# Kernel tuning notes

Measured on AMD Instinct MI355X. Metric: run time of the kernel, lower is better.

The kernel has to match this reference:

```python
import jax, jax.numpy as jnp
import numpy as np

SOS, EOS, PAD = 1, 2, 0


def setup_inputs() -> dict:
    key = jax.random.key(0)
    ks = jax.random.split(key, 8)
    n, d_z, d_h, d_emb, V = 8192, 128, 512, 128, 64
    s = lambda k, shape, scale: jax.random.normal(k, shape, jnp.float32) * scale
    return {
        "Z": jax.random.normal(ks[0], (n, d_z), jnp.float32),
        "emb": s(ks[1], (V, d_emb), 0.1),
        "z2h_w": s(ks[2], (d_h, d_z), 0.05),
        "z2h_b": jnp.zeros((d_h,), jnp.float32),
        "w_ih0": s(ks[3], (3 * d_h, d_emb), 0.05),
        "w_ih_rest": s(ks[4], (2, 3 * d_h, d_h), 0.05),
        "w_hh": s(ks[5], (3, 3 * d_h, d_h), 0.05),
        "b_ih": jnp.zeros((3, 3 * d_h), jnp.float32),
        "b_hh": jnp.zeros((3, 3 * d_h), jnp.float32),
        "h2v_w": s(ks[6], (V, d_h), 0.05),
        "h2v_b": jnp.zeros((V,), jnp.float32),
        "max_len": 80,
    }


def _gru_cell(x, h, w_ih, w_hh, b_ih, b_hh):
    # torch GRU gate order: r, z, n
    gi = x @ w_ih.T + b_ih
    gh = h @ w_hh.T + b_hh
    i_r, i_z, i_n = jnp.split(gi, 3, axis=-1)
    h_r, h_z, h_n = jnp.split(gh, 3, axis=-1)
    r = jax.nn.sigmoid(i_r + h_r)
    z = jax.nn.sigmoid(i_z + h_z)
    g = jnp.tanh(i_n + r * h_n)
    return (1.0 - z) * g + z * h


def _decode(Z, emb, z2h_w, z2h_b, w_ih0, w_ih_rest, w_hh, b_ih, b_hh, h2v_w, h2v_b, max_len):
    n = Z.shape[0]
    L = w_hh.shape[0]
    h0 = Z @ z2h_w.T + z2h_b                      # [n, d_h], repeated over layers
    H = jnp.broadcast_to(h0[None], (L,) + h0.shape)
    x0 = jnp.full((n,), SOS, jnp.int32)
    eos0 = jnp.zeros((n,), bool)
    w_ih = [w_ih0] + [w_ih_rest[i] for i in range(w_ih_rest.shape[0])]

    def step(carry, t):
        H, x_prev, eos = carry
        inp = emb[x_prev]                          # [n, d_emb]
        Hs = []
        for l in range(L):                         # small fixed layer loop
            h_new = _gru_cell(inp, H[l], w_ih[l], w_hh[l], b_ih[l], b_hh[l])
            Hs.append(h_new)
            inp = h_new
        probs = jax.nn.softmax(inp @ h2v_w.T + h2v_b, axis=-1)  # [n, V]
        x_t = jnp.argmax(probs, axis=-1).astype(jnp.int32)      # ModeSampler
        tok = jnp.where(eos, PAD, x_t)             # masked write into X_gen
        new_eos = (~eos) & (x_t == EOS)
        return (jnp.stack(Hs), x_t, eos | new_eos), (tok, new_eos, probs)

    ts = jnp.arange(1, max_len, dtype=jnp.int32)
    _, (toks, new_eos, probs) = jax.lax.scan(step, (H, x0, eos0), ts)
    X_gen = jnp.concatenate([jnp.full((n, 1), SOS, jnp.int32), toks.T], axis=1)  # [n, max_len]
    any_eos = new_eos.any(axis=0)
    first_t = ts[jnp.argmax(new_eos, axis=0)]
    seq_lens = jnp.where(any_eos, first_t + 1, max_len).astype(jnp.int32)
    return X_gen, seq_lens, probs


def reference(Z, emb, z2h_w, z2h_b, w_ih0, w_ih_rest, w_hh, b_ih, b_hh, h2v_w, h2v_b, max_len):
    X_gen, seq_lens, _ = _decode(Z, emb, z2h_w, z2h_b, w_ih0, w_ih_rest,
                                 w_hh, b_ih, b_hh, h2v_w, h2v_b, max_len)
    # torch returns a ragged list X_gen[i, :seq_lens[i]]; we return the padded
    # tensor plus lengths (jit-compatible equivalent).
    return X_gen, seq_lens
```

## Files before the change

### kernel.cpp

```cpp
#include <hip/hip_runtime.h>
#include <math.h>

#define NSEQ 8192
#define DH 512
#define DZ 128
#define DE 128
#define VOCAB 64
#define TMAX 80
#define SOS 1
#define EOS_TOK 2

#define TMR 64
#define TNCOL 32

typedef _Float16 half_t;
typedef half_t h8 __attribute__((ext_vector_type(8)));
typedef float f4 __attribute__((ext_vector_type(4)));

__device__ __forceinline__ float sigf(float x) { return 1.0f / (1.0f + expf(-x)); }

__device__ __forceinline__ void split2(float v, half_t& hi, half_t& lo) {
    float hf = (float)(half_t)v;
    if (fabsf(v) < 6.2e-5f) hf = 0.0f;
    hi = (half_t)hf;
    lo = (half_t)((v - hf) * 2048.0f);
}

__device__ __forceinline__ float rec2(half_t h, half_t l) {
    return (float)h + (float)l * (1.0f / 2048.0f);
}

__device__ __forceinline__ void gl_lds16(const void* g, void* l) {
    __builtin_amdgcn_global_load_lds((const __attribute__((address_space(1))) void*)g,
                                     (__attribute__((address_space(3))) void*)l, 16, 0, 0);
}

__device__ __forceinline__ void swizzle_rc(int bid, int& r, int& c) {
    const int x = bid & 7;
    const int q = bid >> 3;
    r = (q & 15) * 8 + x;
    c = q >> 4;
}

__global__ __launch_bounds__(256) void init_kernel(int* __restrict__ x_prev,
                                                   int* __restrict__ eos,
                                                   int* __restrict__ out,
                                                   int* __restrict__ list0,
                                                   int* __restrict__ counts) {
    int i = blockIdx.x * 256 + threadIdx.x;
    x_prev[i] = SOS;
    eos[i] = 0;
    list0[i] = i;
    out[i * TMAX] = SOS;
    out[NSEQ * TMAX + i] = TMAX;
    if (i < TMAX) counts[i] = (i == 0) ? NSEQ : 0;
}

__global__ __launch_bounds__(256) void h0_kernel(const float* __restrict__ Z,
                                                 const float* __restrict__ w,
                                                 const float* __restrict__ b,
                                                 half_t* __restrict__ B0h, half_t* __restrict__ B0l,
                                                 half_t* __restrict__ B1h, half_t* __restrict__ B1l,
                                                 half_t* __restrict__ B2h, half_t* __restrict__ B2l) {
    __shared__ float zrow[DZ];
    const int i = blockIdx.x;
    const int tid = threadIdx.x;
    if (tid < DZ) zrow[tid] = Z[(size_t)i * DZ + tid];
    __syncthreads();
    for (int j = tid; j < DH; j += 256) {
        double s = (double)b[j];
        const float* wr = w + (size_t)j * DZ;
#pragma unroll 8
        for (int k = 0; k < DZ; ++k) s += (double)zrow[k] * (double)wr[k];
        float sf = (float)s;
        half_t hi, lo;
        split2(sf, hi, lo);
        size_t o = (size_t)i * DH + j;
        B0h[o] = hi; B0l[o] = lo;
        B1h[o] = hi; B1l[o] = lo;
        B2h[o] = hi; B2l[o] = lo;
    }
}

__global__ __launch_bounds__(256) void gi0_kernel(const float* __restrict__ emb,
                                                  const float* __restrict__ w_ih0,
                                                  const float* __restrict__ b_ih0,
                                                  double* __restrict__ tab) {
    __shared__ float e[DE];
    const int x = blockIdx.x;
    const int tid = threadIdx.x;
    if (tid < DE) e[tid] = emb[(size_t)x * DE + tid];
    __syncthreads();
    for (int j = tid; j < 3 * DH; j += 256) {
        double s = (double)b_ih0[j];
        const float* wr = w_ih0 + (size_t)j * DE;
#pragma unroll 8
        for (int k = 0; k < DE; ++k) s += (double)e[k] * (double)wr[k];
        tab[(size_t)x * 3 * DH + j] = s;
    }
}

__global__ __launch_bounds__(256) void wsplit_kernel(const float* __restrict__ w,
                                                     half_t* __restrict__ hi,
                                                     half_t* __restrict__ lo, int n) {
    int i = blockIdx.x * 256 + threadIdx.x;
    if (i < n) {
        half_t h, l;
        split2(w[i], h, l);
        hi[i] = h; lo[i] = l;
    }
}


__global__ __launch_bounds__(256, 3) void layer0_mfma(
    const half_t* __restrict__ Hch, const half_t* __restrict__ Hcl,
    half_t* __restrict__ Hnh, half_t* __restrict__ Hnl,
    const half_t* __restrict__ Wh, const half_t* __restrict__ Wl,
    const float* __restrict__ b_hh0,
    const double* __restrict__ tab,
    const int* __restrict__ x_prev,
    const int* __restrict__ list, const int* __restrict__ count) {
    int rt, ct;
    swizzle_rc(blockIdx.x, rt, ct);
    const int row0 = rt * TMR;
    const int cnt = count[0];
    if (row0 >= cnt) return;
    const int col0 = ct * TNCOL;

    __shared__ char sm[40960];
    const int tid = threadIdx.x;
    const int lane = tid & 63, w = tid >> 6;
    const int lr = lane & 15, lq = lane >> 4;
    const int wr0 = (w >> 1) * 32, wc0 = (w & 1) * 16;

    int aoff[2], boff[3];
#pragma unroll
    for (int i = 0; i < 2; ++i) {
        int u = i * 256 + tid, r = u >> 3, s = u & 7;
        int rr = row0 + r; if (rr > cnt - 1) rr = cnt - 1;
        aoff[i] = list[rr] * 1024 + ((s ^ (r & 7)) << 4);
    }
#pragma unroll
    for (int j = 0; j < 3; ++j) {
        int u = j * 256 + tid, br = u >> 3, s = u & 7;
        int wr = (br >> 5) * DH + col0 + (br & 31);
        boff[j] = wr * 1024 + ((s ^ (br & 7)) << 4);
    }

    int fa[2][2], fb[3][2];
#pragma unroll
    for (int rf = 0; rf < 2; ++rf)
#pragma unroll
        for (int ks = 0; ks < 2; ++ks) {
            int row = wr0 + rf * 16 + lr;
            int sb = ks * 4 + lq;
            fa[rf][ks] = row * 128 + ((sb ^ (row & 7)) << 4);
        }
#pragma unroll
    for (int g = 0; g < 3; ++g)
#pragma unroll
        for (int ks = 0; ks < 2; ++ks) {
            int br = g * 32 + wc0 + lr;
            int sb = ks * 4 + lq;
            fb[g][ks] = br * 128 + ((sb ^ (br & 7)) << 4);
        }

    f4 hh[2][3] = {}, cc[2][3] = {};
    const char* Ah = (const char*)Hch;
    const char* Al = (const char*)Hcl;
    const char* Bh = (const char*)Wh;
    const char* Bl = (const char*)Wl;

    for (int kc = 0; kc < 8; ++kc) {
        const int kb = kc * 128;
#pragma unroll
        for (int i = 0; i < 2; ++i) {
            gl_lds16(Ah + aoff[i] + kb, sm + (i * 256 + tid) * 16);
            gl_lds16(Al + aoff[i] + kb, sm + 8192 + (i * 256 + tid) * 16);
        }
#pragma unroll
        for (int j = 0; j < 3; ++j) {
            gl_lds16(Bh + boff[j] + kb, sm + 16384 + (j * 256 + tid) * 16);
            gl_lds16(Bl + boff[j] + kb, sm + 28672 + (j * 256 + tid) * 16);
        }
        __syncthreads();
#pragma unroll
        for (int ks = 0; ks < 2; ++ks) {
            h8 a0h = *(const h8*)(sm + fa[0][ks]);
            h8 a0l = *(const h8*)(sm + 8192 + fa[0][ks]);
            h8 a1h = *(const h8*)(sm + fa[1][ks]);
            h8 a1l = *(const h8*)(sm + 8192 + fa[1][ks]);
#pragma unroll
            for (int g = 0; g < 3; ++g) {
                h8 bh = *(const h8*)(sm + 16384 + fb[g][ks]);
                h8 bl = *(const h8*)(sm + 28672 + fb[g][ks]);
                hh[0][g] = __builtin_amdgcn_mfma_f32_16x16x32_f16(a0h, bh, hh[0][g], 0, 0, 0);
                cc[0][g] = __builtin_amdgcn_mfma_f32_16x16x32_f16(a0h, bl, cc[0][g], 0, 0, 0);
                cc[0][g] = __builtin_amdgcn_mfma_f32_16x16x32_f16(a0l, bh, cc[0][g], 0, 0, 0);
                hh[1][g] = __builtin_amdgcn_mfma_f32_16x16x32_f16(a1h, bh, hh[1][g], 0, 0, 0);
                cc[1][g] = __builtin_amdgcn_mfma_f32_16x16x32_f16(a1h, bl, cc[1][g], 0, 0, 0);
                cc[1][g] = __builtin_amdgcn_mfma_f32_16x16x32_f16(a1l, bh, cc[1][g], 0, 0, 0);
            }
        }
        __syncthreads();
    }

    const float inv = 1.0f / 2048.0f;
#pragma unroll
    for (int rf = 0; rf < 2; ++rf) {
        f4 pR = hh[rf][0] + cc[rf][0] * inv;
        f4 pZ = hh[rf][1] + cc[rf][1] * inv;
        f4 pN = hh[rf][2] + cc[rf][2] * inv;
        const int gj = col0 + wc0 + lr;
#pragma unroll
        for (int reg = 0; reg < 4; ++reg) {
            int pos = row0 + wr0 + rf * 16 + lq * 4 + reg;
            if (pos > cnt - 1) pos = cnt - 1;
            const int gi = list[pos];
            const double* tr = tab + (size_t)x_prev[gi] * (3 * DH);
            float xr = (float)(tr[gj] + (double)pR[reg] + (double)b_hh0[gj]);
            float xz = (float)(tr[DH + gj] + (double)pZ[reg] + (double)b_hh0[DH + gj]);
            float hn_pre = pN[reg] + b_hh0[2 * DH + gj];
            float r = sigf(xr), z = sigf(xz);
            float g = tanhf((float)(tr[2 * DH + gj] + (double)r * (double)hn_pre));
            size_t o = (size_t)gi * DH + gj;
            float ho = rec2(Hch[o], Hcl[o]);
            float h = (1.0f - z) * g + z * ho;
            half_t oh, ol;
            split2(h, oh, ol);
            Hnh[o] = oh; Hnl[o] = ol;
        }
    }
}

__global__ __launch_bounds__(256, 3) void layer12_mfma(
    const half_t* __restrict__ Xh, const half_t* __restrict__ Xl,
    const half_t* __restrict__ Hch, const half_t* __restrict__ Hcl,
    half_t* __restrict__ Hnh, half_t* __restrict__ Hnl,
    const half_t* __restrict__ Wih_h, const half_t* __restrict__ Wih_l,
    const half_t* __restrict__ Whh_h, const half_t* __restrict__ Whh_l,
    const float* __restrict__ b_ih, const float* __restrict__ b_hh,
    const int* __restrict__ list, const int* __restrict__ count) {
    int rt, ct;
    swizzle_rc(blockIdx.x, rt, ct);
    const int row0 = rt * TMR;
    const int cnt = count[0];
    if (row0 >= cnt) return;
    const int col0 = ct * TNCOL;

    __shared__ char sm[40960];
    const int tid = threadIdx.x;
    const int lane = tid & 63, w = tid >> 6;
    const int lr = lane & 15, lq = lane >> 4;
    const int wr0 = (w >> 1) * 32, wc0 = (w & 1) * 16;

    int aoff[2], boff[3];
#pragma unroll
    for (int i = 0; i < 2; ++i) {
        int u = i * 256 + tid, r = u >> 3, s = u & 7;
        int rr = row0 + r; if (rr > cnt - 1) rr = cnt - 1;
        aoff[i] = list[rr] * 1024 + ((s ^ (r & 7)) << 4);
    }
#pragma unroll
    for (int j = 0; j < 3; ++j) {
        int u = j * 256 + tid, br = u >> 3, s = u & 7;
        int wr = (br >> 5) * DH + col0 + (br & 31);
        boff[j] = wr * 1024 + ((s ^ (br & 7)) << 4);
    }

    int fa[2][2], fb[3][2];
#pragma unroll
    for (int rf = 0; rf < 2; ++rf)
#pragma unroll
        for (int ks = 0; ks < 2; ++ks) {
            int row = wr0 + rf * 16 + lr;
            int sb = ks * 4 + lq;
            fa[rf][ks] = row * 128 + ((sb ^ (row & 7)) << 4);
        }
#pragma unroll
    for (int g = 0; g < 3; ++g)
#pragma unroll
        for (int ks = 0; ks < 2; ++ks) {
            int br = g * 32 + wc0 + lr;
            int sb = ks * 4 + lq;
            fb[g][ks] = br * 128 + ((sb ^ (br & 7)) << 4);
        }

    f4 hh[2][3] = {}, cc[2][3] = {}, niS[2] = {};

    for (int kc = 0; kc < 16; ++kc) {
        const int kb = (kc & 7) * 128;
        const char* As_h = (kc < 8) ? (const char*)Xh : (const char*)Hch;
        const char* As_l = (kc < 8) ? (const char*)Xl : (const char*)Hcl;
        const char* Ws_h = (kc < 8) ? (const char*)Wih_h : (const char*)Whh_h;
        const char* Ws_l = (kc < 8) ? (const char*)Wih_l : (const char*)Whh_l;
#pragma unroll
        for (int i = 0; i < 2; ++i) {
            gl_lds16(As_h + aoff[i] + kb, sm + (i * 256 + tid) * 16);
            gl_lds16(As_l + aoff[i] + kb, sm + 8192 + (i * 256 + tid) * 16);
        }
#pragma unroll
        for (int j = 0; j < 3; ++j) {
            gl_lds16(Ws_h + boff[j] + kb, sm + 16384 + (j * 256 + tid) * 16);
            gl_lds16(Ws_l + boff[j] + kb, sm + 28672 + (j * 256 + tid) * 16);
        }
        __syncthreads();
#pragma unroll
        for (int ks = 0; ks < 2; ++ks) {
            h8 a0h = *(const h8*)(sm + fa[0][ks]);
            h8 a0l = *(const h8*)(sm + 8192 + fa[0][ks]);
            h8 a1h = *(const h8*)(sm + fa[1][ks]);
            h8 a1l = *(const h8*)(sm + 8192 + fa[1][ks]);
#pragma unroll
            for (int g = 0; g < 3; ++g) {
                h8 bh = *(const h8*)(sm + 16384 + fb[g][ks]);
                h8 bl = *(const h8*)(sm + 28672 + fb[g][ks]);
                hh[0][g] = __builtin_amdgcn_mfma_f32_16x16x32_f16(a0h, bh, hh[0][g], 0, 0, 0);
                cc[0][g] = __builtin_amdgcn_mfma_f32_16x16x32_f16(a0h, bl, cc[0][g], 0, 0, 0);
                cc[0][g] = __builtin_amdgcn_mfma_f32_16x16x32_f16(a0l, bh, cc[0][g], 0, 0, 0);
                hh[1][g] = __builtin_amdgcn_mfma_f32_16x16x32_f16(a1h, bh, hh[1][g], 0, 0, 0);
                cc[1][g] = __builtin_amdgcn_mfma_f32_16x16x32_f16(a1h, bl, cc[1][g], 0, 0, 0);
                cc[1][g] = __builtin_amdgcn_mfma_f32_16x16x32_f16(a1l, bh, cc[1][g], 0, 0, 0);
            }
        }
        __syncthreads();
        if (kc == 7) {
#pragma unroll
            for (int rf = 0; rf < 2; ++rf) {
                niS[rf] = hh[rf][2] + cc[rf][2] * (1.0f / 2048.0f);
                f4 zz = {0.0f, 0.0f, 0.0f, 0.0f};
                hh[rf][2] = zz;
                cc[rf][2] = zz;
            }
        }
    }

    const float inv = 1.0f / 2048.0f;
#pragma unroll
    for (int rf = 0; rf < 2; ++rf) {
        f4 pR = hh[rf][0] + cc[rf][0] * inv;
        f4 pZ = hh[rf][1] + cc[rf][1] * inv;
        f4 pNH = hh[rf][2] + cc[rf][2] * inv;
        f4 pNI = niS[rf];
        const int gj = col0 + wc0 + lr;
#pragma unroll
        for (int reg = 0; reg < 4; ++reg) {
            int pos = row0 + wr0 + rf * 16 + lq * 4 + reg;
            if (pos > cnt - 1) pos = cnt - 1;
            const int gi = list[pos];
            float xr = pR[reg] + b_ih[gj] + b_hh[gj];
            float xz = pZ[reg] + b_ih[DH + gj] + b_hh[DH + gj];
            float xi = pNI[reg] + b_ih[2 * DH + gj];
            float hn_pre = pNH[reg] + b_hh[2 * DH + gj];
            float r = sigf(xr), z = sigf(xz);
            float g = tanhf(xi + r * hn_pre);
            size_t o = (size_t)gi * DH + gj;
            float ho = rec2(Hch[o], Hcl[o]);
            float h = (1.0f - z) * g + z * ho;
            half_t oh, ol;
            split2(h, oh, ol);
            Hnh[o] = oh; Hnl[o] = ol;
        }
    }
}

__global__ __launch_bounds__(256) void logits_kernel(const half_t* __restrict__ H2h,
                                                     const half_t* __restrict__ H2l,
                                                     const float* __restrict__ h2v_w,
                                                     const float* __restrict__ h2v_b,
                                                     int* __restrict__ x_prev,
                                                     int* __restrict__ eos,
                                                     int* __restrict__ out,
                                                     const int* __restrict__ list,
                                                     const int* __restrict__ count,
                                                     int* __restrict__ list_next,
                                                     int* __restrict__ count_next,
                                                     int t) {
    const int rowbase = blockIdx.x * 16;
    const int cnt = count[0];
    if (rowbase >= cnt) return;

    __shared__ float Ws[VOCAB][65];
    __shared__ float Hs[16][65];
    __shared__ int sact[16];
    const int tid = threadIdx.x;
    double acc[4] = {0.0, 0.0, 0.0, 0.0};

    for (int k0 = 0; k0 < DH; k0 += 64) {
        __syncthreads();
#pragma unroll
        for (int it = 0; it < 16; ++it) {
            int idx = tid + 256 * it;
            int v = idx >> 6, k = idx & 63;
            Ws[v][k] = h2v_w[(size_t)v * DH + k0 + k];
        }
#pragma unroll
        for (int it = 0; it < 4; ++it) {
            int idx = tid + 256 * it;
            int r = idx >> 6, k = idx & 63;
            int pos = rowbase + r; if (pos > cnt - 1) pos = cnt - 1;
            size_t o = (size_t)list[pos] * DH + k0 + k;
            Hs[r][k] = rec2(H2h[o], H2l[o]);
        }
        __syncthreads();
        const int r = tid >> 4;
        const int vb = (tid & 15) * 4;
#pragma unroll 16
        for (int k = 0; k < 64; ++k) {
            double h = (double)Hs[r][k];
            acc[0] += h * (double)Ws[vb + 0][k];
            acc[1] += h * (double)Ws[vb + 1][k];
            acc[2] += h * (double)Ws[vb + 2][k];
            acc[3] += h * (double)Ws[vb + 3][k];
        }
    }

    const int r = tid >> 4;
    const int vb = (tid & 15) * 4;
    float lf[4];
#pragma unroll
    for (int vv = 0; vv < 4; ++vv) lf[vv] = (float)(acc[vv] + (double)h2v_b[vb + vv]);

    float m = fmaxf(fmaxf(lf[0], lf[1]), fmaxf(lf[2], lf[3]));
#pragma unroll
    for (int off = 1; off < 16; off <<= 1) m = fmaxf(m, __shfl_xor(m, off));
    float e[4];
    float ssum = 0.f;
#pragma unroll
    for (int vv = 0; vv < 4; ++vv) { e[vv] = expf(lf[vv] - m); ssum += e[vv]; }
#pragma unroll
    for (int off = 1; off < 16; off <<= 1) ssum += __shfl_xor(ssum, off);

    float best = e[0] / ssum;
    int bi = vb;
#pragma unroll
    for (int vv = 1; vv < 4; ++vv) {
        float pv = e[vv] / ssum;
        if (pv > best) { best = pv; bi = vb + vv; }
    }
#pragma unroll
    for (int off = 1; off < 16; off <<= 1) {
        float ov = __shfl_xor(best, off);
        int oi = __shfl_xor(bi, off);
        if (ov > best || (ov == best && oi < bi)) { best = ov; bi = oi; }
    }
    if ((tid & 15) == 0) {
        const int pos = rowbase + r;
        const bool valid = pos < cnt;
        const int gi = list[valid ? pos : (cnt - 1)];
        const int ee = eos[gi];
        const int xt = bi;
        if (valid) {
            out[(size_t)gi * TMAX + t] = ee ? 0 : xt;
            if (!ee && xt == EOS_TOK) {
                out[NSEQ * TMAX + gi] = t + 1;
                eos[gi] = 1;
            }
            x_prev[gi] = xt;
        }
        sact[r] = (valid && !ee && xt != EOS_TOK) ? gi : -1;
    }
    __syncthreads();
    if (tid == 0) {
        int loc[16], k = 0;
#pragma unroll
        for (int i = 0; i < 16; ++i) { int v = sact[i]; if (v >= 0) loc[k++] = v; }
        if (k > 0) {
            int b = atomicAdd(count_next, k);
            for (int i = 0; i < k; ++i) list_next[b + i] = loc[i];
        }
    }
}

extern "C" void kernel_launch(void* const* d_in, const int* in_sizes, int n_in,
                              void* d_out, int out_size, void* d_ws, size_t ws_size,
                              hipStream_t stream) {
    const float* Z        = (const float*)d_in[0];
    const float* emb      = (const float*)d_in[1];
    const float* z2h_w    = (const float*)d_in[2];
    const float* z2h_b    = (const float*)d_in[3];
    const float* w_ih0    = (const float*)d_in[4];
    const float* w_ih_rest= (const float*)d_in[5];
    const float* w_hh     = (const float*)d_in[6];
    const float* b_ih     = (const float*)d_in[7];
    const float* b_hh     = (const float*)d_in[8];
    const float* h2v_w    = (const float*)d_in[9];
    const float* h2v_b    = (const float*)d_in[10];

    int* out = (int*)d_out;
    char* p = (char*)d_ws;
    const size_t HS = (size_t)NSEQ * DH * sizeof(half_t);
    half_t* Bh[4]; half_t* Bl[4];
    for (int i = 0; i < 4; ++i) { Bh[i] = (half_t*)p; p += HS; }
    for (int i = 0; i < 4; ++i) { Bl[i] = (half_t*)p; p += HS; }
    double* tab = (double*)p; p += (size_t)VOCAB * 3 * DH * sizeof(double);
    const size_t WH = (size_t)3 * DH * DH;
    half_t* wih_h = (half_t*)p; p += 2 * WH * sizeof(half_t);
    half_t* wih_l = (half_t*)p; p += 2 * WH * sizeof(half_t);
    half_t* whh_h = (half_t*)p; p += 3 * WH * sizeof(half_t);
    half_t* whh_l = (half_t*)p; p += 3 * WH * sizeof(half_t);
    int* x_prev = (int*)p; p += NSEQ * sizeof(int);
    int* eos    = (int*)p; p += NSEQ * sizeof(int);
    int* lists[2];
    lists[0] = (int*)p; p += NSEQ * sizeof(int);
    lists[1] = (int*)p; p += NSEQ * sizeof(int);
    int* counts = (int*)p; p += 128 * sizeof(int);

    hipMemsetAsync(out, 0, (size_t)NSEQ * TMAX * sizeof(int), stream);
    init_kernel<<<NSEQ / 256, 256, 0, stream>>>(x_prev, eos, out, lists[0], counts);
    h0_kernel<<<NSEQ, 256, 0, stream>>>(Z, z2h_w, z2h_b,
                                        Bh[0], Bl[0], Bh[1], Bl[1], Bh[2], Bl[2]);
    gi0_kernel<<<VOCAB, 256, 0, stream>>>(emb, w_ih0, b_ih, tab);
    wsplit_kernel<<<(int)((2 * WH + 255) / 256), 256, 0, stream>>>(w_ih_rest, wih_h, wih_l, (int)(2 * WH));
    wsplit_kernel<<<(int)((3 * WH + 255) / 256), 256, 0, stream>>>(w_hh, whh_h, whh_l, (int)(3 * WH));

    int c0 = 0, c1 = 1, c2 = 2, sp = 3;
    const int lgrid = (NSEQ / TMR) * (DH / TNCOL);
    for (int t = 1; t < TMAX; ++t) {
        const int* lcur = lists[(t - 1) & 1];
        const int* ccur = counts + (t - 1);
        layer0_mfma<<<lgrid, 256, 0, stream>>>(Bh[c0], Bl[c0], Bh[sp], Bl[sp],
            whh_h, whh_l, b_hh, tab, x_prev, lcur, ccur);
        layer12_mfma<<<lgrid, 256, 0, stream>>>(Bh[sp], Bl[sp], Bh[c1], Bl[c1], Bh[c0], Bl[c0],
            wih_h, wih_l, whh_h + WH, whh_l + WH, b_ih + 3 * DH, b_hh + 3 * DH, lcur, ccur);
        layer12_mfma<<<lgrid, 256, 0, stream>>>(Bh[c0], Bl[c0], Bh[c2], Bl[c2], Bh[c1], Bl[c1],
            wih_h + WH, wih_l + WH, whh_h + 2 * WH, whh_l + 2 * WH,
            b_ih + 6 * DH, b_hh + 6 * DH, lcur, ccur);
        logits_kernel<<<NSEQ / 16, 256, 0, stream>>>(Bh[c1], Bl[c1], h2v_w, h2v_b,
                                                     x_prev, eos, out, lcur, ccur,
                                                     lists[t & 1], counts + t, t);
        int n0 = sp, n1 = c0, n2 = c1, nsp = c2;
        c0 = n0; c1 = n1; c2 = n2; sp = nsp;
    }
}
```

Baseline: 14.82 ms.

## Double row tile to 128 and interleave hi/lo halves in one LDS tile

Row tile per block grows from 64 to 128, so each wave computes 4 row fragments and reuses each loaded B fragment across more MFMAs. The K chunk shrinks to 32 elements and hi/lo fp16 parts are packed into the same swizzled LDS row, which cuts shared memory from 40KB to 28KB and halves the number of global-to-LDS copy instructions per chunk. In exchange the kernel runs twice as many K iterations with their barriers, needs more accumulator registers (occupancy bound lowered to 2 blocks), and launches half as many row blocks, which hurts load balance when the active count is small.

Measured after the change: 18.69 ms. 26.2% more time.

```diff
diff --git a/kernel.cpp b/kernel.cpp
--- a/kernel.cpp
+++ b/kernel.cpp
@@ -10,7 +10,7 @@
 #define SOS 1
 #define EOS_TOK 2
 
-#define TMR 64
+#define TMR 128
 #define TNCOL 32
 
 typedef _Float16 half_t;
@@ -38,8 +38,8 @@
 __device__ __forceinline__ void swizzle_rc(int bid, int& r, int& c) {
     const int x = bid & 7;
     const int q = bid >> 3;
-    r = (q & 15) * 8 + x;
-    c = q >> 4;
+    r = (q & 7) * 8 + x;
+    c = q >> 3;
 }
 
 __global__ __launch_bounds__(256) void init_kernel(int* __restrict__ x_prev,
@@ -112,7 +112,7 @@
 }
 
 
-__global__ __launch_bounds__(256, 3) void layer0_mfma(
+__global__ __launch_bounds__(256, 2) void layer0_mfma(
     const half_t* __restrict__ Hch, const half_t* __restrict__ Hcl,
     half_t* __restrict__ Hnh, half_t* __restrict__ Hnl,
     const half_t* __restrict__ Wh, const half_t* __restrict__ Wl,
@@ -127,91 +127,85 @@
     if (row0 >= cnt) return;
     const int col0 = ct * TNCOL;
 
-    __shared__ char sm[40960];
+    __shared__ __align__(16) char sm[28672];
     const int tid = threadIdx.x;
     const int lane = tid & 63, w = tid >> 6;
     const int lr = lane & 15, lq = lane >> 4;
-    const int wr0 = (w >> 1) * 32, wc0 = (w & 1) * 16;
-
-    int aoff[2], boff[3];
-#pragma unroll
-    for (int i = 0; i < 2; ++i) {
-        int u = i * 256 + tid, r = u >> 3, s = u & 7;
+    const int wr0 = (w >> 1) * 64, wc0 = (w & 1) * 16;
+
+    int aoff[4], ahi[4];
+#pragma unroll
+    for (int i = 0; i < 4; ++i) {
+        int u = i * 256 + tid, r = u >> 3, p = u & 7;
+        int l = p ^ (r & 7);
         int rr = row0 + r; if (rr > cnt - 1) rr = cnt - 1;
-        aoff[i] = list[rr] * 1024 + ((s ^ (r & 7)) << 4);
-    }
+        aoff[i] = list[rr] * 1024 + (l & 3) * 16;
+        ahi[i] = (l < 4);
+    }
+    int boff[3], bhi[3];
 #pragma unroll
     for (int j = 0; j < 3; ++j) {
-        int u = j * 256 + tid, br = u >> 3, s = u & 7;
-        int wr = (br >> 5) * DH + col0 + (br & 31);
-        boff[j] = wr * 1024 + ((s ^ (br & 7)) << 4);
-    }
-
-    int fa[2][2], fb[3][2];
-#pragma unroll
-    for (int rf = 0; rf < 2; ++rf)
-#pragma unroll
-        for (int ks = 0; ks < 2; ++ks) {
-            int row = wr0 + rf * 16 + lr;
-            int sb = ks * 4 + lq;
-            fa[rf][ks] = row * 128 + ((sb ^ (row & 7)) << 4);
-        }
-#pragma unroll
-    for (int g = 0; g < 3; ++g)
-#pragma unroll
-        for (int ks = 0; ks < 2; ++ks) {
-            int br = g * 32 + wc0 + lr;
-            int sb = ks * 4 + lq;
-            fb[g][ks] = br * 128 + ((sb ^ (br & 7)) << 4);
-        }
-
-    f4 hh[2][3] = {}, cc[2][3] = {};
-    const char* Ah = (const char*)Hch;
-    const char* Al = (const char*)Hcl;
-    const char* Bh = (const char*)Wh;
-    const char* Bl = (const char*)Wl;
-
-    for (int kc = 0; kc < 8; ++kc) {
-        const int kb = kc * 128;
-#pragma unroll
-        for (int i = 0; i < 2; ++i) {
-            gl_lds16(Ah + aoff[i] + kb, sm + (i * 256 + tid) * 16);
-            gl_lds16(Al + aoff[i] + kb, sm + 8192 + (i * 256 + tid) * 16);
-        }
-#pragma unroll
-        for (int j = 0; j < 3; ++j) {
-            gl_lds16(Bh + boff[j] + kb, sm + 16384 + (j * 256 + tid) * 16);
-            gl_lds16(Bl + boff[j] + kb, sm + 28672 + (j * 256 + tid) * 16);
-        }
+        int u = j * 256 + tid, r = u >> 3, p = u & 7;
+        int l = p ^ (r & 7);
+        int wr = (r >> 5) * DH + col0 + (r & 31);
+        boff[j] = wr * 1024 + (l & 3) * 16;
+        bhi[j] = (l < 4);
+    }
+
+    int fah[4], fal[4], fbh[3], fbl[3];
+#pragma unroll
+    for (int rf = 0; rf < 4; ++rf) {
+        int arow = wr0 + rf * 16 + lr;
+        fah[rf] = arow * 128 + ((lq ^ (arow & 7)) << 4);
+        fal[rf] = arow * 128 + (((lq ^ 4) ^ (arow & 7)) << 4);
+    }
+#pragma unroll
+    for (int g = 0; g < 3; ++g) {
+        int brow = g * 32 + wc0 + lr;
+        fbh[g] = 16384 + brow * 128 + ((lq ^ (brow & 7)) << 4);
+        fbl[g] = 16384 + brow * 128 + (((lq ^ 4) ^ (brow & 7)) << 4);
+    }
+
+    f4 hh[4][3] = {}, cc[4][3] = {};
+
+    for (int kc = 0; kc < 16; ++kc) {
+        const int kb = kc * 64;
+#pragma unroll
+        for (int i = 0; i < 4; ++i)
+            gl_lds16((ahi[i] ? (const char*)Hch : (const char*)Hcl) + aoff[i] + kb,
+                     sm + (i * 256 + tid) * 16);
+#pragma unroll
+        for (int j = 0; j < 3; ++j)
+            gl_lds16((bhi[j] ? (const char*)Wh : (const char*)Wl) + boff[j] + kb,
+                     sm + 16384 + (j * 256 + tid) * 16);
         __syncthreads();
-#pragma unroll
-        for (int ks = 0; ks < 2; ++ks) {
-            h8 a0h = *(const h8*)(sm + fa[0][ks]);
-            h8 a0l = *(const h8*)(sm + 8192 + fa[0][ks]);
-            h8 a1h = *(const h8*)(sm + fa[1][ks]);
-            h8 a1l = *(const h8*)(sm + 8192 + fa[1][ks]);
-#pragma unroll
-            for (int g = 0; g < 3; ++g) {
-                h8 bh = *(const h8*)(sm + 16384 + fb[g][ks]);
-                h8 bl = *(const h8*)(sm + 28672 + fb[g][ks]);
-                hh[0][g] = __builtin_amdgcn_mfma_f32_16x16x32_f16(a0h, bh, hh[0][g], 0, 0, 0);
-                cc[0][g] = __builtin_amdgcn_mfma_f32_16x16x32_f16(a0h, bl, cc[0][g], 0, 0, 0);
-                cc[0][g] = __builtin_amdgcn_mfma_f32_16x16x32_f16(a0l, bh, cc[0][g], 0, 0, 0);
-                hh[1][g] = __builtin_amdgcn_mfma_f32_16x16x32_f16(a1h, bh, hh[1][g], 0, 0, 0);
-                cc[1][g] = __builtin_amdgcn_mfma_f32_16x16x32_f16(a1h, bl, cc[1][g], 0, 0, 0);
-                cc[1][g] = __builtin_amdgcn_mfma_f32_16x16x32_f16(a1l, bh, cc[1][g], 0, 0, 0);
+        h8 ah[4], al[4];
+#pragma unroll
+        for (int rf = 0; rf < 4; ++rf) {
+            ah[rf] = *(const h8*)(sm + fah[rf]);
+            al[rf] = *(const h8*)(sm + fal[rf]);
+        }
+#pragma unroll
+        for (int g = 0; g < 3; ++g) {
+            h8 bh = *(const h8*)(sm + fbh[g]);
+            h8 bl = *(const h8*)(sm + fbl[g]);
+#pragma unroll
+            for (int rf = 0; rf < 4; ++rf) {
+                hh[rf][g] = __builtin_amdgcn_mfma_f32_16x16x32_f16(ah[rf], bh, hh[rf][g], 0, 0, 0);
+                cc[rf][g] = __builtin_amdgcn_mfma_f32_16x16x32_f16(ah[rf], bl, cc[rf][g], 0, 0, 0);
+                cc[rf][g] = __builtin_amdgcn_mfma_f32_16x16x32_f16(al[rf], bh, cc[rf][g], 0, 0, 0);
             }
         }
         __syncthreads();
     }
 
     const float inv = 1.0f / 2048.0f;
-#pragma unroll
-    for (int rf = 0; rf < 2; ++rf) {
+    const int gj = col0 + wc0 + lr;
+#pragma unroll
+    for (int rf = 0; rf < 4; ++rf) {
         f4 pR = hh[rf][0] + cc[rf][0] * inv;
         f4 pZ = hh[rf][1] + cc[rf][1] * inv;
         f4 pN = hh[rf][2] + cc[rf][2] * inv;
-        const int gj = col0 + wc0 + lr;
 #pragma unroll
         for (int reg = 0; reg < 4; ++reg) {
             int pos = row0 + wr0 + rf * 16 + lq * 4 + reg;
@@ -233,7 +227,7 @@
     }
 }
 
-__global__ __launch_bounds__(256, 3) void layer12_mfma(
+__global__ __launch_bounds__(256, 2) void layer12_mfma(
     const half_t* __restrict__ Xh, const half_t* __restrict__ Xl,
     const half_t* __restrict__ Hch, const half_t* __restrict__ Hcl,
     half_t* __restrict__ Hnh, half_t* __restrict__ Hnl,
@@ -248,85 +242,81 @@
     if (row0 >= cnt) return;
     const int col0 = ct * TNCOL;
 
-    __shared__ char sm[40960];
+    __shared__ __align__(16) char sm[28672];
     const int tid = threadIdx.x;
     const int lane = tid & 63, w = tid >> 6;
     const int lr = lane & 15, lq = lane >> 4;
-    const int wr0 = (w >> 1) * 32, wc0 = (w & 1) * 16;
-
-    int aoff[2], boff[3];
-#pragma unroll
-    for (int i = 0; i < 2; ++i) {
-        int u = i * 256 + tid, r = u >> 3, s = u & 7;
+    const int wr0 = (w >> 1) * 64, wc0 = (w & 1) * 16;
+
+    int aoff[4], ahi[4];
+#pragma unroll
+    for (int i = 0; i < 4; ++i) {
+        int u = i * 256 + tid, r = u >> 3, p = u & 7;
+        int l = p ^ (r & 7);
         int rr = row0 + r; if (rr > cnt - 1) rr = cnt - 1;
-        aoff[i] = list[rr] * 1024 + ((s ^ (r & 7)) << 4);
-    }
+        aoff[i] = list[rr] * 1024 + (l & 3) * 16;
+        ahi[i] = (l < 4);
+    }
+    int boff[3], bhi[3];
 #pragma unroll
     for (int j = 0; j < 3; ++j) {
-        int u = j * 256 + tid, br = u >> 3, s = u & 7;
-        int wr = (br >> 5) * DH + col0 + (br & 31);
-        boff[j] = wr * 1024 + ((s ^ (br & 7)) << 4);
-    }
-
-    int fa[2][2], fb[3][2];
-#pragma unroll
-    for (int rf = 0; rf < 2; ++rf)
-#pragma unroll
-        for (int ks = 0; ks < 2; ++ks) {
-            int row = wr0 + rf * 16 + lr;
-            int sb = ks * 4 + lq;
-            fa[rf][ks] = row * 128 + ((sb ^ (row & 7)) << 4);
-        }
-#pragma unroll
-    for (int g = 0; g < 3; ++g)
-#pragma unroll
-        for (int ks = 0; ks < 2; ++ks) {
-            int br = g * 32 + wc0 + lr;
-            int sb = ks * 4 + lq;
-            fb[g][ks] = br * 128 + ((sb ^ (br & 7)) << 4);
-        }
-
-    f4 hh[2][3] = {}, cc[2][3] = {}, niS[2] = {};
-
-    for (int kc = 0; kc < 16; ++kc) {
-        const int kb = (kc & 7) * 128;
-        const char* As_h = (kc < 8) ? (const char*)Xh : (const char*)Hch;
-        const char* As_l = (kc < 8) ? (const char*)Xl : (const char*)Hcl;
-        const char* Ws_h = (kc < 8) ? (const char*)Wih_h : (const char*)Whh_h;
-        const char* Ws_l = (kc < 8) ? (const char*)Wih_l : (const char*)Whh_l;
-#pragma unroll
-        for (int i = 0; i < 2; ++i) {
-            gl_lds16(As_h + aoff[i] + kb, sm + (i * 256 + tid) * 16);
-            gl_lds16(As_l + aoff[i] + kb, sm + 8192 + (i * 256 + tid) * 16);
-        }
-#pragma unroll
-        for (int j = 0; j < 3; ++j) {
-            gl_lds16(Ws_h + boff[j] + kb, sm + 16384 + (j * 256 + tid) * 16);
-            gl_lds16(Ws_l + boff[j] + kb, sm + 28672 + (j * 256 + tid) * 16);
-        }
+        int u = j * 256 + tid, r = u >> 3, p = u & 7;
+        int l = p ^ (r & 7);
+        int wr = (r >> 5) * DH + col0 + (r & 31);
+        boff[j] = wr * 1024 + (l & 3) * 16;
+        bhi[j] = (l < 4);
+    }
+
+    int fah[4], fal[4], fbh[3], fbl[3];
+#pragma unroll
+    for (int rf = 0; rf < 4; ++rf) {
+        int arow = wr0 + rf * 16 + lr;
+        fah[rf] = arow * 128 + ((lq ^ (arow & 7)) << 4);
+        fal[rf] = arow * 128 + (((lq ^ 4) ^ (arow & 7)) << 4);
+    }
+#pragma unroll
+    for (int g = 0; g < 3; ++g) {
+        int brow = g * 32 + wc0 + lr;
+        fbh[g] = 16384 + brow * 128 + ((lq ^ (brow & 7)) << 4);
+        fbl[g] = 16384 + brow * 128 + (((lq ^ 4) ^ (brow & 7)) << 4);
+    }
+
+    f4 hh[4][3] = {}, cc[4][3] = {}, niS[4] = {};
+
+    for (int kc = 0; kc < 32; ++kc) {
+        const int kb = (kc & 15) * 64;
+        const char* Ah_ = (kc < 16) ? (const char*)Xh : (const char*)Hch;
+        const char* Al_ = (kc < 16) ? (const char*)Xl : (const char*)Hcl;
+        const char* Wh_ = (kc < 16) ? (const char*)Wih_h : (const char*)Whh_h;
+        const char* Wl_ = (kc < 16) ? (const char*)Wih_l : (const char*)Whh_l;
+#pragma unroll
+        for (int i = 0; i < 4; ++i)
+            gl_lds16((ahi[i] ? Ah_ : Al_) + aoff[i] + kb, sm + (i * 256 + tid) * 16);
+#pragma unroll
+        for (int j = 0; j < 3; ++j)
+            gl_lds16((bhi[j] ? Wh_ : Wl_) + boff[j] + kb, sm + 16384 + (j * 256 + tid) * 16);
         __syncthreads();
-#pragma unroll
-        for (int ks = 0; ks < 2; ++ks) {
-            h8 a0h = *(const h8*)(sm + fa[0][ks]);
-            h8 a0l = *(const h8*)(sm + 8192 + fa[0][ks]);
-            h8 a1h = *(const h8*)(sm + fa[1][ks]);
-            h8 a1l = *(const h8*)(sm + 8192 + fa[1][ks]);
-#pragma unroll
-            for (int g = 0; g < 3; ++g) {
-                h8 bh = *(const h8*)(sm + 16384 + fb[g][ks]);
-                h8 bl = *(const h8*)(sm + 28672 + fb[g][ks]);
-                hh[0][g] = __builtin_amdgcn_mfma_f32_16x16x32_f16(a0h, bh, hh[0][g], 0, 0, 0);
-                cc[0][g] = __builtin_amdgcn_mfma_f32_16x16x32_f16(a0h, bl, cc[0][g], 0, 0, 0);
-                cc[0][g] = __builtin_amdgcn_mfma_f32_16x16x32_f16(a0l, bh, cc[0][g], 0, 0, 0);
-                hh[1][g] = __builtin_amdgcn_mfma_f32_16x16x32_f16(a1h, bh, hh[1][g], 0, 0, 0);
-                cc[1][g] = __builtin_amdgcn_mfma_f32_16x16x32_f16(a1h, bl, cc[1][g], 0, 0, 0);
-                cc[1][g] = __builtin_amdgcn_mfma_f32_16x16x32_f16(a1l, bh, cc[1][g], 0, 0, 0);
+        h8 ah[4], al[4];
+#pragma unroll
+        for (int rf = 0; rf < 4; ++rf) {
+            ah[rf] = *(const h8*)(sm + fah[rf]);
+            al[rf] = *(const h8*)(sm + fal[rf]);
+        }
+#pragma unroll
+        for (int g = 0; g < 3; ++g) {
+            h8 bh = *(const h8*)(sm + fbh[g]);
+            h8 bl = *(const h8*)(sm + fbl[g]);
+#pragma unroll
+            for (int rf = 0; rf < 4; ++rf) {
+                hh[rf][g] = __builtin_amdgcn_mfma_f32_16x16x32_f16(ah[rf], bh, hh[rf][g], 0, 0, 0);
+                cc[rf][g] = __builtin_amdgcn_mfma_f32_16x16x32_f16(ah[rf], bl, cc[rf][g], 0, 0, 0);
+                cc[rf][g] = __builtin_amdgcn_mfma_f32_16x16x32_f16(al[rf], bh, cc[rf][g], 0, 0, 0);
             }
         }
         __syncthreads();
-        if (kc == 7) {
-#pragma unroll
-            for (int rf = 0; rf < 2; ++rf) {
+        if (kc == 15) {
+#pragma unroll
+            for (int rf = 0; rf < 4; ++rf) {
                 niS[rf] = hh[rf][2] + cc[rf][2] * (1.0f / 2048.0f);
                 f4 zz = {0.0f, 0.0f, 0.0f, 0.0f};
                 hh[rf][2] = zz;
@@ -336,13 +326,13 @@
     }
 
     const float inv = 1.0f / 2048.0f;
-#pragma unroll
-    for (int rf = 0; rf < 2; ++rf) {
+    const int gj = col0 + wc0 + lr;
+#pragma unroll
+    for (int rf = 0; rf < 4; ++rf) {
         f4 pR = hh[rf][0] + cc[rf][0] * inv;
         f4 pZ = hh[rf][1] + cc[rf][1] * inv;
         f4 pNH = hh[rf][2] + cc[rf][2] * inv;
         f4 pNI = niS[rf];
-        const int gj = col0 + wc0 + lr;
 #pragma unroll
         for (int reg = 0; reg < 4; ++reg) {
             int pos = row0 + wr0 + rf * 16 + lq * 4 + reg;
```
